# Kernel optimization log

Measured on AMD Instinct MI355X. Metric: run time of the kernel, lower is better.

## Reference

```python
import jax, jax.numpy as jnp
import numpy as np

NUM_EMBEDDINGS = 1024
EMBEDDING_DIM = 256
COMMITMENT_COST = 0.25


def setup_inputs() -> dict:
    key = jax.random.key(0)
    k_z, k_e = jax.random.split(key)
    z = jax.random.normal(k_z, (8, EMBEDDING_DIM, 16, 16, 16), dtype=jnp.float32)
    # nn.Embedding weight initialized uniform(-1/K, 1/K)
    codebook = jax.random.uniform(
        k_e, (NUM_EMBEDDINGS, EMBEDDING_DIM), dtype=jnp.float32,
        minval=-1.0 / NUM_EMBEDDINGS, maxval=1.0 / NUM_EMBEDDINGS)
    return {"z": z, "codebook": codebook}


def reference(z, codebook):
    B, D, H, W, L = z.shape
    # (B, D, H, W, L) -> (B, H, W, L, D) -> (N, D)
    z_perm = jnp.transpose(z, (0, 2, 3, 4, 1))          # (B,H,W,L,D)
    z_flat = z_perm.reshape(-1, D)                       # (N,D)
    # squared-distance via expansion: ||z||^2 + ||e||^2 - 2 z.e^T
    distances = ((z_flat ** 2).sum(axis=1, keepdims=True)
                 + (codebook ** 2).sum(axis=1)
                 - 2.0 * z_flat @ codebook.T)            # (N,K)
    indices = jnp.argmin(distances, axis=1)              # (N,)
    quantized = codebook[indices].reshape(B, H, W, L, D)
    idx_out = indices.reshape(B, H, W, L)
    # losses (stop_gradient mirrors .detach())
    e_latent_loss = jnp.mean((jax.lax.stop_gradient(quantized) - z_perm) ** 2)
    q_latent_loss = jnp.mean((quantized - jax.lax.stop_gradient(z_perm)) ** 2)
    vq_loss = q_latent_loss + COMMITMENT_COST * e_latent_loss
    # straight-through estimator
    quant_st = z_perm + jax.lax.stop_gradient(quantized - z_perm)
    quant_out = jnp.transpose(quant_st, (0, 4, 1, 2, 3))  # (B,D,H,W,L)
    return quant_out, idx_out, vq_loss
```

## Files before the change

kernel.cpp:

```cpp
#include <hip/hip_runtime.h>


#define K_CODES 1024
#define DIM 256
#define N_TOK 32768
#define SPATIAL 4096
#define TOK_BLK 64
#define NBLK (N_TOK / TOK_BLK)
#define CAP 28
#define MARGIN 1e-3f
#define ZLD 257

typedef __attribute__((ext_vector_type(8))) short short8;
typedef __attribute__((ext_vector_type(4))) float float4v;

#define WS_LOSS 0
#define WS_CNT 8
#define WS_E2 16
#define WS_EB 2048
#define WS_SZ 133120
#define WS_CAND 165888
#define WS_CCNT 624640

#define O_IDX (8 * DIM * SPATIAL)
#define O_LOSS (O_IDX + N_TOK)

__device__ __forceinline__ short f2bf(float v) {
  unsigned u = __float_as_uint(v);
  u = (u + 0x7fffu + ((u >> 16) & 1u)) >> 16;
  return (short)u;
}

__global__ __launch_bounds__(256) void prep_kernel(const float* __restrict__ e,
                                                   float* __restrict__ ws) {
  __shared__ float sq[DIM];
  __shared__ __align__(16) short sbf[DIM];
  __shared__ float chv[16];
  int k = blockIdx.x, d = threadIdx.x;
  float v = e[k * DIM + d];
  sbf[d] = f2bf(v);
  sq[d] = __fmul_rn(v, v);
  __syncthreads();
  if (d < 32) {
    int f = d >> 2, q = d & 3;
    int stage = k >> 6, ct = (k >> 4) & 3, nn = k & 15;
    short8 chunk = *(const short8*)(sbf + f * 32 + q * 8);
    int off8 = ((stage * 4 + ct) * 8 + f) * 64 + q * 16 + nn;
    ((short8*)(ws + WS_EB))[off8] = chunk;
  }
  if (d < 16) {
    int blkb = d >> 3, j = d & 7;
    const float* x = sq + blkb * 128;
    float c = x[j];
#pragma unroll
    for (int i = 1; i < 16; i++) c = __fadd_rn(c, x[i * 8 + j]);
    chv[d] = c;
  }
  __syncthreads();
  if (d == 0) {
    float a0 = __fadd_rn(__fadd_rn(chv[0], chv[1]), __fadd_rn(chv[2], chv[3]));
    float a1 = __fadd_rn(__fadd_rn(chv[4], chv[5]), __fadd_rn(chv[6], chv[7]));
    float resA = __fadd_rn(a0, a1);
    float b0 = __fadd_rn(__fadd_rn(chv[8], chv[9]), __fadd_rn(chv[10], chv[11]));
    float b1 = __fadd_rn(__fadd_rn(chv[12], chv[13]), __fadd_rn(chv[14], chv[15]));
    float resB = __fadd_rn(b0, b1);
    ws[WS_E2 + k] = __fadd_rn(resA, resB);
    if (k == 0) {
      ws[WS_LOSS] = 0.f;
      ((unsigned*)ws)[WS_CNT] = 0u;
    }
  }
}

__global__ __launch_bounds__(512, 4) void filter_kernel(const float* __restrict__ z,
                                                        float* __restrict__ ws) {
  __shared__ __align__(16) short Bst[64 * 256];
  __shared__ unsigned short cand[TOK_BLK][CAP];
  __shared__ int cnt[TOK_BLK];
  __shared__ float Szp[2][TOK_BLK];

  int tid = threadIdx.x, w = tid >> 6, lane = tid & 63;
  int quad = lane >> 4, nn = lane & 15;
  int g = w & 3, kh = w >> 2;
  int n0 = blockIdx.x * TOK_BLK;
  int b = n0 >> 12, s0 = n0 & 4095;
  const float* zb = z + (size_t)b * DIM * SPATIAL + s0;
  const float* Se = ws + WS_E2;
  const uint4* eBg = (const uint4*)(ws + WS_EB);
  if (tid < TOK_BLK) cnt[tid] = 0;

  {
    const float* zp = zb + g * 16 + nn;
    float r0, r1;
    {
      int j0 = quad * 2;
      float v0 = zp[(size_t)(kh * 128 + j0) * SPATIAL];
      float v1 = zp[(size_t)(kh * 128 + j0 + 1) * SPATIAL];
      r0 = __fmul_rn(v0, v0);
      r1 = __fmul_rn(v1, v1);
      for (int i = 1; i < 16; i++) {
        v0 = zp[(size_t)(kh * 128 + i * 8 + j0) * SPATIAL];
        v1 = zp[(size_t)(kh * 128 + i * 8 + j0 + 1) * SPATIAL];
        r0 = __fadd_rn(r0, __fmul_rn(v0, v0));
        r1 = __fadd_rn(r1, __fmul_rn(v1, v1));
      }
    }
    float p = __fadd_rn(r0, r1);
    float s1 = __fadd_rn(p, __shfl_xor(p, 16));
    float s2 = __fadd_rn(s1, __shfl_xor(s1, 32));
    if (quad == 0) Szp[kh][g * 16 + nn] = s2;
  }

  int tokA = g * 16 + nn;
  short8 A[8];
#pragma unroll
  for (int f = 0; f < 8; f++) {
    short8 a;
#pragma unroll
    for (int j = 0; j < 8; j++) {
      int d = f * 32 + quad * 8 + j;
      a[j] = f2bf(zb[(size_t)d * SPATIAL + tokA]);
    }
    A[f] = a;
  }

  float thr[4] = {3.4e38f, 3.4e38f, 3.4e38f, 3.4e38f};
  for (int stage = 0; stage < 16; stage++) {
    __syncthreads();
#pragma unroll
    for (int i = 0; i < 4; i++)
      ((uint4*)Bst)[i * 512 + tid] = eBg[(size_t)stage * 2048 + i * 512 + tid];
    __syncthreads();

    int ct0 = kh * 2, ct1 = kh * 2 + 1;
    int kbase0 = stage * 64 + ct0 * 16;
    int kbase1 = stage * 64 + ct1 * 16;
    float4v C0 = {0.f, 0.f, 0.f, 0.f};
    float4v C1 = {0.f, 0.f, 0.f, 0.f};
    const short8* Bp0 = (const short8*)Bst + ct0 * 8 * 64;
    const short8* Bp1 = (const short8*)Bst + ct1 * 8 * 64;
#pragma unroll
    for (int f = 0; f < 8; f++) {
      short8 B0 = Bp0[f * 64 + lane];
      short8 B1 = Bp1[f * 64 + lane];
      C0 = __builtin_amdgcn_mfma_f32_16x16x32_bf16(A[f], B0, C0, 0, 0, 0);
      C1 = __builtin_amdgcn_mfma_f32_16x16x32_bf16(A[f], B1, C1, 0, 0, 0);
    }
    float SeK0 = Se[kbase0 + nn];
    float SeK1 = Se[kbase1 + nn];
    float s0v[4], s1v[4], m0[4], m1[4];
#pragma unroll
    for (int r = 0; r < 4; r++) {
      s0v[r] = fmaf(-2.f, C0[r], SeK0);
      s1v[r] = fmaf(-2.f, C1[r], SeK1);
      m0[r] = s0v[r];
      m1[r] = s1v[r];
    }
#pragma unroll
    for (int dlt = 1; dlt <= 8; dlt <<= 1) {
#pragma unroll
      for (int r = 0; r < 4; r++) {
        m0[r] = fminf(m0[r], __shfl_xor(m0[r], dlt, 16));
        m1[r] = fminf(m1[r], __shfl_xor(m1[r], dlt, 16));
      }
    }
    bool pr[4];
#pragma unroll
    for (int r = 0; r < 4; r++) {
      thr[r] = fminf(thr[r], m0[r]);
      pr[r] = s0v[r] < thr[r] + MARGIN;
    }
    if (__ballot(pr[0] | pr[1] | pr[2] | pr[3])) {
#pragma unroll
      for (int r = 0; r < 4; r++) {
        unsigned long long bl = __ballot(pr[r]);
        unsigned grp = (unsigned)((bl >> (quad * 16)) & 0xffffULL);
        if (grp) {
          int tb = g * 16 + quad * 4 + r;
          int base = 0;
          if (nn == 0) base = atomicAdd(&cnt[tb], __popc(grp));
          base = __shfl(base, quad * 16);
          if (pr[r]) {
            int pos = base + __popc(grp & ((1u << nn) - 1u));
            if (pos < CAP) cand[tb][pos] = (unsigned short)(kbase0 + nn);
          }
        }
      }
    }
#pragma unroll
    for (int r = 0; r < 4; r++) {
      thr[r] = fminf(thr[r], m1[r]);
      pr[r] = s1v[r] < thr[r] + MARGIN;
    }
    if (__ballot(pr[0] | pr[1] | pr[2] | pr[3])) {
#pragma unroll
      for (int r = 0; r < 4; r++) {
        unsigned long long bl = __ballot(pr[r]);
        unsigned grp = (unsigned)((bl >> (quad * 16)) & 0xffffULL);
        if (grp) {
          int tb = g * 16 + quad * 4 + r;
          int base = 0;
          if (nn == 0) base = atomicAdd(&cnt[tb], __popc(grp));
          base = __shfl(base, quad * 16);
          if (pr[r]) {
            int pos = base + __popc(grp & ((1u << nn) - 1u));
            if (pos < CAP) cand[tb][pos] = (unsigned short)(kbase1 + nn);
          }
        }
      }
    }
  }
  __syncthreads();

  {
    int t = tid >> 3, j = tid & 7;
    int cv = cnt[t];
    if (j == 0) ((int*)ws)[WS_CCNT + n0 + t] = cv;
    if (j == 1)
      ws[WS_SZ + n0 + t] = __fadd_rn(Szp[0][t], Szp[1][t]);
    int cl = cv < CAP ? cv : CAP;
    unsigned short* cg = (unsigned short*)(ws + WS_CAND) + (size_t)(n0 + t) * CAP;
    for (int c = j; c < cl; c += 8) cg[c] = cand[t][c];
  }
}

__global__ __launch_bounds__(512, 4) void de_kernel(const float* __restrict__ z,
                                                    const float* __restrict__ e,
                                                    float* __restrict__ ws,
                                                    float* __restrict__ out) {
  __shared__ float zs[TOK_BLK * ZLD];
  __shared__ int mini_sh[TOK_BLK];
  __shared__ float red[8];

  int tid = threadIdx.x, w = tid >> 6, lane = tid & 63;
  int n0 = blockIdx.x * TOK_BLK;
  int b = n0 >> 12, s0 = n0 & 4095;
  const float* zb = z + (size_t)b * DIM * SPATIAL + s0;
  const float* Se = ws + WS_E2;
  const unsigned short* candg = (const unsigned short*)(ws + WS_CAND);
  const int* cntg = (const int*)ws + WS_CCNT;

#pragma unroll
  for (int it = 0; it < 8; it++) {
    int c = it * 512 + tid;
    int d = c >> 4, t4 = (c & 15) << 2;
    float4 v4 = *(const float4*)(zb + (size_t)d * SPATIAL + t4);
    zs[(t4 + 0) * ZLD + d] = v4.x;
    zs[(t4 + 1) * ZLD + d] = v4.y;
    zs[(t4 + 2) * ZLD + d] = v4.z;
    zs[(t4 + 3) * ZLD + d] = v4.w;
  }
  __syncthreads();

  int tl = lane >> 3, oct = lane & 7;
  int tb = w * 8 + tl;
  int tok = n0 + tb;
  int cc = cntg[tok];
  int cl = cc < CAP ? cc : CAP;
  float Szn = ws[WS_SZ + tok];
  float bestD = 3.4e38f;
  int bestk = 0x7fffffff;
  {
    const float* zp = zs + tb * ZLD;
    const unsigned short* cg = candg + (size_t)tok * CAP;
    for (int c = oct; c < cl; c += 8) {
      int k = cg[c];
      const float* er = e + (size_t)k * DIM;
      float acc = 0.f;
#pragma unroll 4
      for (int dd = 0; dd < DIM; dd += 4) {
        float4 e4 = *(const float4*)(er + dd);
        acc = fmaf(zp[dd + 0], e4.x, acc);
        acc = fmaf(zp[dd + 1], e4.y, acc);
        acc = fmaf(zp[dd + 2], e4.z, acc);
        acc = fmaf(zp[dd + 3], e4.w, acc);
      }
      float D = __fsub_rn(__fadd_rn(Szn, Se[k]), __fmul_rn(2.f, acc));
      if (D < bestD || (D == bestD && k < bestk)) { bestD = D; bestk = k; }
    }
  }
#pragma unroll
  for (int off = 4; off >= 1; off >>= 1) {
    float oD = __shfl_down(bestD, off, 8);
    int ok = __shfl_down(bestk, off, 8);
    if (oD < bestD || (oD == bestD && ok < bestk)) { bestD = oD; bestk = ok; }
  }
  if (oct == 0 && cc <= CAP) {
    mini_sh[tb] = bestk;
    out[O_IDX + tok] = (float)bestk;
  }
  for (int t = 0; t < 8; t++) {
    int tb2 = w * 8 + t;
    if (cntg[n0 + tb2] > CAP) {
      const float* zq = zs + tb2 * ZLD;
      float Sz2 = ws[WS_SZ + n0 + tb2];
      float bD = 3.4e38f;
      int bk = 0x7fffffff;
      for (int k = lane; k < K_CODES; k += 64) {
        const float* er = e + (size_t)k * DIM;
        float acc = 0.f;
#pragma unroll 4
        for (int dd = 0; dd < DIM; dd += 4) {
          float4 e4 = *(const float4*)(er + dd);
          acc = fmaf(zq[dd + 0], e4.x, acc);
          acc = fmaf(zq[dd + 1], e4.y, acc);
          acc = fmaf(zq[dd + 2], e4.z, acc);
          acc = fmaf(zq[dd + 3], e4.w, acc);
        }
        float D = __fsub_rn(__fadd_rn(Sz2, Se[k]), __fmul_rn(2.f, acc));
        if (D < bD || (D == bD && k < bk)) { bD = D; bk = k; }
      }
#pragma unroll
      for (int m = 1; m < 64; m <<= 1) {
        float oD = __shfl_xor(bD, m);
        int ok = __shfl_xor(bk, m);
        if (oD < bD || (oD == bD && ok < bk)) { bD = oD; bk = ok; }
      }
      if (lane == 0) {
        mini_sh[tb2] = bk;
        out[O_IDX + n0 + tb2] = (float)bk;
      }
    }
  }
  __syncthreads();

  int mten = mini_sh[lane];
  const float* erow = e + (size_t)mten * DIM;
  const float* zrow = zs + lane * ZLD;
  float* op = out + (size_t)b * DIM * SPATIAL + s0;
  float sumsq = 0.f;
#pragma unroll 2
  for (int i4 = 0; i4 < 32; i4 += 4) {
    int d = w * 32 + i4;
    float4 v4 = *(const float4*)(erow + d);
#pragma unroll
    for (int m = 0; m < 4; m++) {
      float v = (m == 0) ? v4.x : (m == 1) ? v4.y : (m == 2) ? v4.z : v4.w;
      float zv = zrow[d + m];
      float df = __fsub_rn(v, zv);
      sumsq = fmaf(df, df, sumsq);
      op[(size_t)(d + m) * SPATIAL + lane] = v;
    }
  }
#pragma unroll
  for (int o = 32; o > 0; o >>= 1) sumsq += __shfl_down(sumsq, o, 64);
  if (lane == 0) red[w] = sumsq;
  __syncthreads();
  if (tid == 0) {
    float rs = ((red[0] + red[1]) + (red[2] + red[3])) +
               ((red[4] + red[5]) + (red[6] + red[7]));
    atomicAdd(ws + WS_LOSS, rs);
    __threadfence();
    unsigned t = atomicAdd((unsigned*)ws + WS_CNT, 1u);
    if (t == NBLK - 1) {
      float total = atomicAdd(ws + WS_LOSS, 0.f);
      out[O_LOSS] = 1.25f * total / 8388608.f;
    }
  }
}

extern "C" void kernel_launch(void* const* d_in, const int* in_sizes, int n_in,
                              void* d_out, int out_size, void* d_ws, size_t ws_size,
                              hipStream_t stream) {
  const float* z = (const float*)d_in[0];
  const float* e = (const float*)d_in[1];
  float* ws = (float*)d_ws;
  float* out = (float*)d_out;

  prep_kernel<<<K_CODES, 256, 0, stream>>>(e, ws);
  filter_kernel<<<NBLK, 512, 0, stream>>>(z, ws);
  de_kernel<<<NBLK, 512, 0, stream>>>(z, e, ws, out);
}
```

Measured before the change: 205.2 us.

## Flatten candidate refinement into block-wide work list with atomicMin argmin

Replaces the fixed 8-lanes-per-token candidate loop and separate per-warp full-codebook fallback with a flattened work list: a serial prefix sum over per-token candidate counts (fallback tokens get all 1024 codes), then each of 512 threads binary-searches its token and computes one exact dot product, combining results through a 64-bit packed shared-memory atomicMin. This balances uneven candidate counts across the block and spreads overflow tokens over all threads. It adds a serial prefix scan by one thread, extra syncs, and shared atomics, and loses the coalesced per-warp access pattern of the fallback path.

```diff
diff --git a/kernel.cpp b/kernel.cpp
--- a/kernel.cpp
+++ b/kernel.cpp
@@ -29,6 +29,12 @@
   unsigned u = __float_as_uint(v);
   u = (u + 0x7fffu + ((u >> 16) & 1u)) >> 16;
   return (short)u;
+}
+
+__device__ __forceinline__ unsigned long long packDK(float D, int k) {
+  unsigned ds = __float_as_uint(D);
+  unsigned key = (ds & 0x80000000u) ? ~ds : (ds ^ 0x80000000u);
+  return ((unsigned long long)key << 32) | (unsigned)k;
 }
 
 __global__ __launch_bounds__(256) void prep_kernel(const float* __restrict__ e,
@@ -229,6 +235,10 @@
                                                     float* __restrict__ ws,
                                                     float* __restrict__ out) {
   __shared__ float zs[TOK_BLK * ZLD];
+  __shared__ unsigned long long best[TOK_BLK];
+  __shared__ int pre[TOK_BLK + 1];
+  __shared__ int cntl[TOK_BLK];
+  __shared__ float Szs[TOK_BLK];
   __shared__ int mini_sh[TOK_BLK];
   __shared__ float red[8];
 
@@ -250,77 +260,49 @@
     zs[(t4 + 2) * ZLD + d] = v4.z;
     zs[(t4 + 3) * ZLD + d] = v4.w;
   }
-  __syncthreads();
-
-  int tl = lane >> 3, oct = lane & 7;
-  int tb = w * 8 + tl;
-  int tok = n0 + tb;
-  int cc = cntg[tok];
-  int cl = cc < CAP ? cc : CAP;
-  float Szn = ws[WS_SZ + tok];
-  float bestD = 3.4e38f;
-  int bestk = 0x7fffffff;
-  {
-    const float* zp = zs + tb * ZLD;
-    const unsigned short* cg = candg + (size_t)tok * CAP;
-    for (int c = oct; c < cl; c += 8) {
-      int k = cg[c];
-      const float* er = e + (size_t)k * DIM;
-      float acc = 0.f;
+  if (tid < TOK_BLK) {
+    int cc = cntg[n0 + tid];
+    cntl[tid] = cc;
+    pre[tid] = (cc > CAP) ? K_CODES : cc;
+    Szs[tid] = ws[WS_SZ + n0 + tid];
+    best[tid] = 0xFFFFFFFFFFFFFFFFULL;
+  }
+  __syncthreads();
+  if (tid == 0) {
+    int s = 0;
+    for (int t = 0; t < TOK_BLK; t++) { int v = pre[t]; pre[t] = s; s += v; }
+    pre[TOK_BLK] = s;
+  }
+  __syncthreads();
+  int T = pre[TOK_BLK];
+
+  for (int i = tid; i < T; i += 512) {
+    int lo = 0, hi = TOK_BLK - 1;
+    while (lo < hi) {
+      int mid = (lo + hi + 1) >> 1;
+      if (pre[mid] <= i) lo = mid; else hi = mid - 1;
+    }
+    int t = lo, j = i - pre[t];
+    int k = (cntl[t] > CAP) ? j : (int)candg[(size_t)(n0 + t) * CAP + j];
+    const float* er = e + (size_t)k * DIM;
+    const float* zp = zs + t * ZLD;
+    float acc = 0.f;
 #pragma unroll 4
-      for (int dd = 0; dd < DIM; dd += 4) {
-        float4 e4 = *(const float4*)(er + dd);
-        acc = fmaf(zp[dd + 0], e4.x, acc);
-        acc = fmaf(zp[dd + 1], e4.y, acc);
-        acc = fmaf(zp[dd + 2], e4.z, acc);
-        acc = fmaf(zp[dd + 3], e4.w, acc);
-      }
-      float D = __fsub_rn(__fadd_rn(Szn, Se[k]), __fmul_rn(2.f, acc));
-      if (D < bestD || (D == bestD && k < bestk)) { bestD = D; bestk = k; }
-    }
-  }
-#pragma unroll
-  for (int off = 4; off >= 1; off >>= 1) {
-    float oD = __shfl_down(bestD, off, 8);
-    int ok = __shfl_down(bestk, off, 8);
-    if (oD < bestD || (oD == bestD && ok < bestk)) { bestD = oD; bestk = ok; }
-  }
-  if (oct == 0 && cc <= CAP) {
-    mini_sh[tb] = bestk;
-    out[O_IDX + tok] = (float)bestk;
-  }
-  for (int t = 0; t < 8; t++) {
-    int tb2 = w * 8 + t;
-    if (cntg[n0 + tb2] > CAP) {
-      const float* zq = zs + tb2 * ZLD;
-      float Sz2 = ws[WS_SZ + n0 + tb2];
-      float bD = 3.4e38f;
-      int bk = 0x7fffffff;
-      for (int k = lane; k < K_CODES; k += 64) {
-        const float* er = e + (size_t)k * DIM;
-        float acc = 0.f;
-#pragma unroll 4
-        for (int dd = 0; dd < DIM; dd += 4) {
-          float4 e4 = *(const float4*)(er + dd);
-          acc = fmaf(zq[dd + 0], e4.x, acc);
-          acc = fmaf(zq[dd + 1], e4.y, acc);
-          acc = fmaf(zq[dd + 2], e4.z, acc);
-          acc = fmaf(zq[dd + 3], e4.w, acc);
-        }
-        float D = __fsub_rn(__fadd_rn(Sz2, Se[k]), __fmul_rn(2.f, acc));
-        if (D < bD || (D == bD && k < bk)) { bD = D; bk = k; }
-      }
-#pragma unroll
-      for (int m = 1; m < 64; m <<= 1) {
-        float oD = __shfl_xor(bD, m);
-        int ok = __shfl_xor(bk, m);
-        if (oD < bD || (oD == bD && ok < bk)) { bD = oD; bk = ok; }
-      }
-      if (lane == 0) {
-        mini_sh[tb2] = bk;
-        out[O_IDX + n0 + tb2] = (float)bk;
-      }
-    }
+    for (int dd = 0; dd < DIM; dd += 4) {
+      float4 e4 = *(const float4*)(er + dd);
+      acc = fmaf(zp[dd + 0], e4.x, acc);
+      acc = fmaf(zp[dd + 1], e4.y, acc);
+      acc = fmaf(zp[dd + 2], e4.z, acc);
+      acc = fmaf(zp[dd + 3], e4.w, acc);
+    }
+    float D = __fsub_rn(__fadd_rn(Szs[t], Se[k]), __fmul_rn(2.f, acc));
+    atomicMin(&best[t], packDK(D, k));
+  }
+  __syncthreads();
+  if (tid < TOK_BLK) {
+    int k = (int)(best[tid] & 0xFFFFFFFFu);
+    mini_sh[tid] = k;
+    out[O_IDX + n0 + tid] = (float)k;
   }
   __syncthreads();
 
```

Measured after the change: 222.9 us. 8.6% more time.
